# Performance work log

Hardware: AMD Instinct MI355X
Metric: run time of the kernel (lower is better)

## Reference

```python
import jax, jax.numpy as jnp
import numpy as np

D = 1024
H = 16
DH = D // H  # 64


def setup_inputs() -> dict:
    key = jax.random.key(0)
    ks = jax.random.split(key, 11)
    B, S = 2, 2048
    s = 1.0 / np.sqrt(D)  # torch Linear default init scale (uniform bound)
    mk = lambda k, shape: jax.random.uniform(k, shape, jnp.float32, -s, s)
    return {
        "q": jax.random.normal(ks[0], (B, S, D), jnp.float32),
        "k": jax.random.normal(ks[1], (B, S, D), jnp.float32),
        "v": jax.random.normal(ks[2], (B, S, D), jnp.float32),
        "Wq": mk(ks[3], (D, D)), "bq": mk(ks[4], (D,)),
        "Wk": mk(ks[5], (D, D)), "bk": mk(ks[6], (D,)),
        "Wv": mk(ks[7], (D, D)), "bv": mk(ks[8], (D,)),
        "Wo": mk(ks[9], (D, D)), "bo": mk(ks[10], (D,)),
    }


def reference(q, k, v, Wq, bq, Wk, bk, Wv, bv, Wo, bo):
    B, S, _ = q.shape
    scaling = DH ** (-0.5)
    # torch Linear: x @ W.T + b ; then split heads -> (B, H, S, DH)
    split = lambda x: x.reshape(B, -1, H, DH).transpose(0, 2, 1, 3)
    Q = split(q @ Wq.T + bq)
    K = split(k @ Wk.T + bk)
    V = split(v @ Wv.T + bv)
    scores = jnp.einsum("bhqd,bhkd->bhqk", Q, K) * scaling  # [B,H,S,S]
    attn = jax.nn.softmax(scores, axis=-1)
    out = jnp.einsum("bhqk,bhkd->bhqd", attn, V)
    out = out.transpose(0, 2, 1, 3).reshape(B, S, D)
    return out @ Wo.T + bo
```

## Files before the change

### kernel.cpp

```cpp
#include <hip/hip_runtime.h>
#include <stdint.h>

#define DIM   1024
#define HEADS 16
#define DHEAD 64
#define SEQ   2048
#define MROWS 4096
#define NQ    (MROWS * DIM)
#define NW    (DIM * DIM)

typedef unsigned short u16;
typedef __attribute__((ext_vector_type(8))) short short8;
typedef __attribute__((ext_vector_type(16))) float f32x16;

static_assert(sizeof(short8) == 16, "short8 must be 16B");

__device__ __forceinline__ float bf2f(u16 u) {
  union { float f; uint32_t u; } x; x.u = ((uint32_t)u) << 16; return x.f;
}
__device__ __forceinline__ u16 f2bf(float f) {
  union { float f; uint32_t u; } x; x.f = f;
  uint32_t r = x.u + 0x7FFFu + ((x.u >> 16) & 1u);
  return (u16)(r >> 16);
}
__device__ __forceinline__ float asf(uint32_t u) {
  union { float f; uint32_t u; } x; x.u = u; return x.f;
}
__device__ __forceinline__ uint32_t cvtpk(float lo, float hi) {
  uint32_t r;
  asm("v_cvt_pk_bf16_f32 %0, %1, %2" : "=v"(r) : "v"(lo), "v"(hi));
  return r;
}
__device__ __forceinline__ float exp2fast(float x) {
#if __has_builtin(__builtin_amdgcn_exp2f)
  return __builtin_amdgcn_exp2f(x);
#else
  return __expf(x * 0.69314718055994531f);
#endif
}

#if __has_builtin(__builtin_amdgcn_global_load_lds)
#define HAVE_GLLDS 1
#else
#define HAVE_GLLDS 0
#endif

__device__ __forceinline__ void stage16(const u16* src, u16* ldsbase, int cb, int lane) {
#if HAVE_GLLDS
  (void)lane;
  __builtin_amdgcn_global_load_lds((const __attribute__((address_space(1))) void*)src,
                                   (__attribute__((address_space(3))) void*)(ldsbase + (size_t)cb * 8),
                                   16, 0, 0);
#else
  *(short8*)(ldsbase + ((size_t)cb + lane) * 8) = *(const short8*)src;
#endif
}

__global__ __launch_bounds__(256)
void cvt_all(const float* __restrict__ q, const float* __restrict__ k, const float* __restrict__ v,
             const float* __restrict__ wq, const float* __restrict__ wk,
             const float* __restrict__ wv, const float* __restrict__ wo,
             u16* __restrict__ qc, u16* __restrict__ kc, u16* __restrict__ vc,
             u16* __restrict__ wqc, u16* __restrict__ wkc, u16* __restrict__ wvc, u16* __restrict__ woc)
{
  const float* s; u16* d; int n;
  switch (blockIdx.y) {
    case 0: s = q;  d = qc;  n = NQ; break;
    case 1: s = k;  d = kc;  n = NQ; break;
    case 2: s = v;  d = vc;  n = NQ; break;
    case 3: s = wq; d = wqc; n = NW; break;
    case 4: s = wk; d = wkc; n = NW; break;
    case 5: s = wv; d = wvc; n = NW; break;
    default: s = wo; d = woc; n = NW; break;
  }
  const int n8 = n >> 3;
  for (int i = blockIdx.x * blockDim.x + threadIdx.x; i < n8; i += gridDim.x * blockDim.x) {
    float4 f0 = ((const float4*)s)[2 * i];
    float4 f1 = ((const float4*)s)[2 * i + 1];
    union { uint32_t w[4]; short8 s8; } u;
    u.w[0] = cvtpk(f0.x, f0.y); u.w[1] = cvtpk(f0.z, f0.w);
    u.w[2] = cvtpk(f1.x, f1.y); u.w[3] = cvtpk(f1.z, f1.w);
    ((short8*)d)[i] = u.s8;
  }
}

__global__ __launch_bounds__(256)
void gemm_qkv(const u16* __restrict__ A0, const u16* __restrict__ W0, const float* __restrict__ b0, u16* __restrict__ O0, float s0_,
              const u16* __restrict__ A1, const u16* __restrict__ W1, const float* __restrict__ b1, u16* __restrict__ O1, float s1_,
              const u16* __restrict__ A2, const u16* __restrict__ W2, const float* __restrict__ b2, u16* __restrict__ O2, float s2_)
{
  constexpr int BM = 128, BN = 128, BK = 64;
  __shared__ u16 As[BM * BK];
  __shared__ u16 Bs[BN * BK];

  const u16* A = A0; const u16* W = W0; const float* bias = b0; u16* O = O0; float oscale = s0_;
  if (blockIdx.z == 1) { A = A1; W = W1; bias = b1; O = O1; oscale = s1_; }
  else if (blockIdx.z == 2) { A = A2; W = W2; bias = b2; O = O2; oscale = s2_; }

  const int tid  = threadIdx.x;
  const int wave = tid >> 6, lane = tid & 63;
  const int l31 = lane & 31, hi = lane >> 5;
  const int wr = wave >> 1, wc = wave & 1;
  const int bx = ((blockIdx.x & 7) << 2) | (blockIdx.x >> 3);
  const int m0 = bx * BM, n0 = blockIdx.y * BN;

  f32x16 acc[2][2];
  for (int mb = 0; mb < 2; ++mb)
    for (int nb = 0; nb < 2; ++nb)
      for (int r = 0; r < 16; ++r) acc[mb][nb][r] = 0.f;

  for (int k0 = 0; k0 < DIM; k0 += BK) {
    __syncthreads();
    constexpr int AI = (BM * 8) / 256;
    for (int i = 0; i < AI; ++i) {
      int cb = (wave * AI + i) * 64;
      int ch = cb + lane;
      int row = ch >> 3, kc = ch & 7;
      stage16(A + (size_t)(m0 + row) * DIM + k0 + (kc ^ (row & 7)) * 8, As, cb, lane);
    }
    constexpr int BI = (BN * 8) / 256;
    for (int i = 0; i < BI; ++i) {
      int cb = (wave * BI + i) * 64;
      int ch = cb + lane;
      int row = ch >> 3, kc = ch & 7;
      stage16(W + (size_t)(n0 + row) * DIM + k0 + (kc ^ (row & 7)) * 8, Bs, cb, lane);
    }
    __syncthreads();

    #pragma unroll
    for (int kk = 0; kk < 4; ++kk) {
      short8 af[2], bf[2];
      #pragma unroll
      for (int mb = 0; mb < 2; ++mb) {
        uint32_t row = (uint32_t)(wr * 64 + mb * 32 + l31);
        af[mb] = *(const short8*)((const char*)As +
                   (row * 128 + ((uint32_t)(kk * 32 + hi * 16) ^ ((row & 7) << 4))));
      }
      #pragma unroll
      for (int nb = 0; nb < 2; ++nb) {
        uint32_t row = (uint32_t)(wc * 64 + nb * 32 + l31);
        bf[nb] = *(const short8*)((const char*)Bs +
                   (row * 128 + ((uint32_t)(kk * 32 + hi * 16) ^ ((row & 7) << 4))));
      }
      __builtin_amdgcn_s_setprio(1);
      #pragma unroll
      for (int mb = 0; mb < 2; ++mb)
        #pragma unroll
        for (int nb = 0; nb < 2; ++nb)
          acc[mb][nb] = __builtin_amdgcn_mfma_f32_32x32x16_bf16(af[mb], bf[nb], acc[mb][nb], 0, 0, 0);
      __builtin_amdgcn_s_setprio(0);
    }
  }

  for (int nb = 0; nb < 2; ++nb) {
    int col = n0 + wc * 64 + nb * 32 + l31;
    float bv = bias[col];
    int hh = col >> 6, dh = col & 63;
    for (int mb = 0; mb < 2; ++mb) {
      int rowb = m0 + wr * 64 + mb * 32 + hi * 4;
      for (int r = 0; r < 16; ++r) {
        int row = rowb + (r & 3) + ((r >> 2) << 3);
        float val = (acc[mb][nb][r] + bv) * oscale;
        int b = row >> 11, s = row & (SEQ - 1);
        O[((((size_t)b * HEADS + hh) * SEQ + s) << 6) + dh] = f2bf(val);
      }
    }
  }
}

__global__ __launch_bounds__(256)
void gemm_out(const u16* __restrict__ Op0, const u16* __restrict__ Op1,
              const float* __restrict__ lstats, const u16* __restrict__ W,
              const float* __restrict__ bias, float* __restrict__ Out)
{
  constexpr int BM = 64, BN = 128, BK = 64;
  __shared__ u16 As[BM * BK];
  __shared__ u16 Bs[BN * BK];
  __shared__ float wtab[HEADS * BM];

  const int tid  = threadIdx.x;
  const int wave = tid >> 6, lane = tid & 63;
  const int l31 = lane & 31, hi = lane >> 5;
  const int wr = wave >> 1, wc = wave & 1;
  const int bx = ((blockIdx.x & 7) << 3) | (blockIdx.x >> 3);
  const int m0 = bx * BM, n0 = blockIdx.y * BN;

  for (int e = tid; e < HEADS * BM; e += 256) {
    int h = e >> 6, r = e & 63;
    int row = m0 + r;
    int b = row >> 11, s = row & (SEQ - 1);
    float l0 = lstats[(size_t)(b * 16 + h) * SEQ + s];
    float l1 = lstats[(size_t)(32 + b * 16 + h) * SEQ + s];
    wtab[e] = 1.0f / (l0 + l1);
  }

  f32x16 acc[2];
  for (int nb = 0; nb < 2; ++nb)
    for (int r = 0; r < 16; ++r) acc[nb][r] = 0.f;

  for (int k0 = 0; k0 < DIM; k0 += BK) {
    __syncthreads();
    const int h = k0 >> 6;
    constexpr int AI = (BM * 8) / 256;
    #pragma unroll
    for (int i = 0; i < AI; ++i) {
      int ch = (wave * AI + i) * 64 + lane;
      int row = ch >> 3, kc = ch & 7;
      int grow = m0 + row;
      int b = grow >> 11, s = grow & (SEQ - 1);
      size_t off = ((size_t)(b * 16 + h) * SEQ + s) * 64 + kc * 8;
      short8 a8 = *(const short8*)(Op0 + off);
      short8 b8 = *(const short8*)(Op1 + off);
      float winv = wtab[h * BM + row];
      union { uint32_t w[4]; short8 s8; } u;
      const uint32_t* wa = (const uint32_t*)&a8;
      const uint32_t* wb = (const uint32_t*)&b8;
      #pragma unroll
      for (int j = 0; j < 4; ++j) {
        float lo = (asf(wa[j] << 16) + asf(wb[j] << 16)) * winv;
        float hi2 = (asf(wa[j] & 0xffff0000u) + asf(wb[j] & 0xffff0000u)) * winv;
        u.w[j] = cvtpk(lo, hi2);
      }
      *(short8*)((char*)As + (((uint32_t)row * 128 + (uint32_t)kc * 16) ^ (((uint32_t)row & 7) << 4))) = u.s8;
    }
    constexpr int BI = (BN * 8) / 256;
    for (int i = 0; i < BI; ++i) {
      int cb = (wave * BI + i) * 64;
      int ch = cb + lane;
      int row = ch >> 3, kc = ch & 7;
      stage16(W + (size_t)(n0 + row) * DIM + k0 + (kc ^ (row & 7)) * 8, Bs, cb, lane);
    }
    __syncthreads();

    #pragma unroll
    for (int kk = 0; kk < 4; ++kk) {
      short8 af, bf[2];
      {
        uint32_t row = (uint32_t)(wr * 32 + l31);
        af = *(const short8*)((const char*)As +
               (row * 128 + ((uint32_t)(kk * 32 + hi * 16) ^ ((row & 7) << 4))));
      }
      #pragma unroll
      for (int nb = 0; nb < 2; ++nb) {
        uint32_t row = (uint32_t)(wc * 64 + nb * 32 + l31);
        bf[nb] = *(const short8*)((const char*)Bs +
                   (row * 128 + ((uint32_t)(kk * 32 + hi * 16) ^ ((row & 7) << 4))));
      }
      __builtin_amdgcn_s_setprio(1);
      #pragma unroll
      for (int nb = 0; nb < 2; ++nb)
        acc[nb] = __builtin_amdgcn_mfma_f32_32x32x16_bf16(af, bf[nb], acc[nb], 0, 0, 0);
      __builtin_amdgcn_s_setprio(0);
    }
  }

  for (int nb = 0; nb < 2; ++nb) {
    int col = n0 + wc * 64 + nb * 32 + l31;
    float bv = bias[col];
    int rowb = m0 + wr * 32 + hi * 4;
    for (int r = 0; r < 16; ++r) {
      int row = rowb + (r & 3) + ((r >> 2) << 3);
      Out[(size_t)row * DIM + col] = acc[nb][r] + bv;
    }
  }
}

#if __has_builtin(__builtin_amdgcn_permlane32_swap)
typedef __attribute__((ext_vector_type(2))) unsigned uint2v;
#define REPACK(PF, A_, B_, C_, D_)                                             \
  {                                                                            \
    uint2v w02 = __builtin_amdgcn_permlane32_swap((A_), (C_), false, false);   \
    uint2v w13 = __builtin_amdgcn_permlane32_swap((B_), (D_), false, false);   \
    union { uint32_t w[4]; short8 s8; } u_;                                    \
    u_.w[0] = w02[0]; u_.w[1] = w13[0]; u_.w[2] = w02[1]; u_.w[3] = w13[1];    \
    PF = u_.s8;                                                                \
  }
#else
#define REPACK(PF, A_, B_, C_, D_)                                             \
  {                                                                            \
    uint32_t pa = __shfl_xor((int)(A_), 32), pb = __shfl_xor((int)(B_), 32);   \
    uint32_t pc = __shfl_xor((int)(C_), 32), pd = __shfl_xor((int)(D_), 32);   \
    union { uint32_t w[4]; short8 s8; } u_;                                    \
    u_.w[0] = hi ? pc : (A_); u_.w[1] = hi ? pd : (B_);                        \
    u_.w[2] = hi ? (C_) : pa; u_.w[3] = hi ? (D_) : pb;                        \
    PF = u_.s8;                                                                \
  }
#endif

#define PV_BLOCK(SS, KSB)                                                      \
  {                                                                            \
    uint32_t a  = cvtpk(SS[0], SS[1]),   b3 = cvtpk(SS[2], SS[3]);             \
    uint32_t c  = cvtpk(SS[4], SS[5]),   d  = cvtpk(SS[6], SS[7]);             \
    uint32_t e  = cvtpk(SS[8], SS[9]),   f  = cvtpk(SS[10], SS[11]);           \
    uint32_t g2 = cvtpk(SS[12], SS[13]), h2 = cvtpk(SS[14], SS[15]);           \
    short8 pf0, pf1;                                                           \
    REPACK(pf0, a, b3, c, d)                                                   \
    REPACK(pf1, e, f, g2, h2)                                                  \
    uint32_t kvb0 = (uint32_t)((KSB) * 64 + hi * 16), kvb1 = kvb0 + 32;        \
    uint32_t r0 = (uint32_t)l31, r1 = 32u + (uint32_t)l31;                     \
    uint32_t sw = ((uint32_t)l31 & 7) << 4;                                    \
    short8 vf00 = *(const short8*)(Vc + ((r0 * 128 + kvb0) ^ sw));             \
    short8 vf01 = *(const short8*)(Vc + ((r1 * 128 + kvb0) ^ sw));             \
    short8 vf10 = *(const short8*)(Vc + ((r0 * 128 + kvb1) ^ sw));             \
    short8 vf11 = *(const short8*)(Vc + ((r1 * 128 + kvb1) ^ sw));             \
    __builtin_amdgcn_s_setprio(1);                                             \
    o0   = __builtin_amdgcn_mfma_f32_32x32x16_bf16(vf00, pf0, o0, 0, 0, 0);    \
    o1   = __builtin_amdgcn_mfma_f32_32x32x16_bf16(vf01, pf0, o1, 0, 0, 0);    \
    accL = __builtin_amdgcn_mfma_f32_32x32x16_bf16(ones8, pf0, accL, 0, 0, 0); \
    o0   = __builtin_amdgcn_mfma_f32_32x32x16_bf16(vf10, pf1, o0, 0, 0, 0);    \
    o1   = __builtin_amdgcn_mfma_f32_32x32x16_bf16(vf11, pf1, o1, 0, 0, 0);    \
    accL = __builtin_amdgcn_mfma_f32_32x32x16_bf16(ones8, pf1, accL, 0, 0, 0); \
    __builtin_amdgcn_s_setprio(0);                                             \
  }

__global__ __launch_bounds__(256)
void attn_fwd7(const u16* __restrict__ Qb, const u16* __restrict__ Kb,
               const u16* __restrict__ Vb, u16* __restrict__ Opart,
               float* __restrict__ lstats)
{
  uint32_t lid = blockIdx.x;
  uint32_t logical = (lid & 7) * 128 + (lid >> 3);
  const int qt    = logical & 15;
  const int bh    = (logical >> 4) & 31;
  const int split = logical >> 9;

  const int q0 = qt * 128;
  const int kvbase = split * (SEQ / 2);
  const int tid = threadIdx.x, wave = tid >> 6, lane = tid & 63;
  const int l31 = lane & 31, hi = lane >> 5;

  const size_t base = (size_t)bh * SEQ * DHEAD;
  const u16* Qg = Qb + base;
  const u16* Kg = Kb + base;
  const u16* Vg = Vb + base;

  __shared__ u16 Ks[2][64 * 64];
  __shared__ u16 Vts[2][64 * 64];

  const short8 ones8 = {0x3F80, 0x3F80, 0x3F80, 0x3F80,
                        0x3F80, 0x3F80, 0x3F80, 0x3F80};

  short8 qf[4];
  {
    const u16* qrow = Qg + (size_t)(q0 + wave * 32 + l31) * DHEAD + hi * 8;
    for (int ks = 0; ks < 4; ++ks)
      qf[ks] = *(const short8*)(qrow + ks * 16);
  }

  f32x16 o0, o1, accL;
  for (int r = 0; r < 16; ++r) { o0[r] = 0.f; o1[r] = 0.f; accL[r] = 0.f; }

  const int rp = tid & 31, c8 = tid >> 5;
  const int kr = tid >> 3, kc0 = tid & 7;
  short8 ka, kb2, va, vb2;

  const u16* pKa = Kg + (size_t)(kvbase + kr) * DHEAD + kc0 * 8;
  const u16* pKb = pKa + 32 * DHEAD;
  const u16* pVa = Vg + (size_t)(kvbase + 2 * rp) * DHEAD + c8 * 8;
  const u16* pVb = pVa + DHEAD;

  {
    ka  = *(const short8*)pKa;
    kb2 = *(const short8*)pKb;
    va  = *(const short8*)pVa;
    vb2 = *(const short8*)pVb;
    uint32_t sw = ((uint32_t)kr & 7) << 4;
    *(short8*)((char*)Ks[0] + (((uint32_t)kr * 128 + (uint32_t)kc0 * 16) ^ sw)) = ka;
    *(short8*)((char*)Ks[0] + ((((uint32_t)kr + 32) * 128 + (uint32_t)kc0 * 16) ^ sw)) = kb2;
    for (int j = 0; j < 8; ++j) {
      uint32_t row = c8 * 8 + j;
      uint32_t byte = (row * 128 + rp * 4) ^ ((row & 7) << 4);
      *(uint32_t*)((char*)Vts[0] + byte) =
          (uint32_t)(u16)va[j] | ((uint32_t)(u16)vb2[j] << 16);
    }
  }
  __syncthreads();

  for (int t = 0; t < 16; ++t) {
    const int cur = t & 1;
    if (t < 15) {
      pKa += 64 * DHEAD; pKb += 64 * DHEAD;
      pVa += 64 * DHEAD; pVb += 64 * DHEAD;
      ka  = *(const short8*)pKa;
      kb2 = *(const short8*)pKb;
      va  = *(const short8*)pVa;
      vb2 = *(const short8*)pVb;
    }

    const char* Kc = (const char*)Ks[cur];
    const char* Vc = (const char*)Vts[cur];

    f32x16 s0, s1;
    for (int r = 0; r < 16; ++r) { s0[r] = 0.f; s1[r] = 0.f; }
    {
      uint32_t rb0 = (uint32_t)l31 * 128, sw0 = ((uint32_t)l31 & 7) << 4;
      uint32_t cbyte = (uint32_t)hi * 16;
      short8 k0 = *(const short8*)(Kc + ((rb0 + cbyte     ) ^ sw0));
      short8 k1 = *(const short8*)(Kc + ((rb0 + cbyte + 32) ^ sw0));
      short8 k2 = *(const short8*)(Kc + ((rb0 + cbyte + 64) ^ sw0));
      short8 k3 = *(const short8*)(Kc + ((rb0 + cbyte + 96) ^ sw0));
      uint32_t rb1 = rb0 + 32 * 128;
      short8 k4 = *(const short8*)(Kc + ((rb1 + cbyte     ) ^ sw0));
      short8 k5 = *(const short8*)(Kc + ((rb1 + cbyte + 32) ^ sw0));
      short8 k6 = *(const short8*)(Kc + ((rb1 + cbyte + 64) ^ sw0));
      short8 k7 = *(const short8*)(Kc + ((rb1 + cbyte + 96) ^ sw0));
      __builtin_amdgcn_s_setprio(1);
      s0 = __builtin_amdgcn_mfma_f32_32x32x16_bf16(k0, qf[0], s0, 0, 0, 0);
      s0 = __builtin_amdgcn_mfma_f32_32x32x16_bf16(k1, qf[1], s0, 0, 0, 0);
      s0 = __builtin_amdgcn_mfma_f32_32x32x16_bf16(k2, qf[2], s0, 0, 0, 0);
      s0 = __builtin_amdgcn_mfma_f32_32x32x16_bf16(k3, qf[3], s0, 0, 0, 0);
      s1 = __builtin_amdgcn_mfma_f32_32x32x16_bf16(k4, qf[0], s1, 0, 0, 0);
      s1 = __builtin_amdgcn_mfma_f32_32x32x16_bf16(k5, qf[1], s1, 0, 0, 0);
      s1 = __builtin_amdgcn_mfma_f32_32x32x16_bf16(k6, qf[2], s1, 0, 0, 0);
      s1 = __builtin_amdgcn_mfma_f32_32x32x16_bf16(k7, qf[3], s1, 0, 0, 0);
      __builtin_amdgcn_s_setprio(0);
    }

    for (int r = 0; r < 16; ++r) s0[r] = exp2fast(s0[r]);
    for (int r = 0; r < 16; ++r) s1[r] = exp2fast(s1[r]);

    PV_BLOCK(s0, 0)
    PV_BLOCK(s1, 1)

    if (t < 15) {
      uint32_t sw = ((uint32_t)kr & 7) << 4;
      char* Kn = (char*)Ks[cur ^ 1];
      *(short8*)(Kn + (((uint32_t)kr * 128 + (uint32_t)kc0 * 16) ^ sw)) = ka;
      *(short8*)(Kn + ((((uint32_t)kr + 32) * 128 + (uint32_t)kc0 * 16) ^ sw)) = kb2;
      char* Vn = (char*)Vts[cur ^ 1];
      for (int j = 0; j < 8; ++j) {
        uint32_t row = c8 * 8 + j;
        uint32_t byte = (row * 128 + rp * 4) ^ ((row & 7) << 4);
        *(uint32_t*)(Vn + byte) =
            (uint32_t)(u16)va[j] | ((uint32_t)(u16)vb2[j] << 16);
      }
      __syncthreads();
    }
  }

  const int q = q0 + wave * 32 + l31;
  u16* orow = Opart + (((size_t)split * 32 + bh) * SEQ + q) * DHEAD;
  for (int db = 0; db < 2; ++db) {
    const f32x16& o = db ? o1 : o0;
    for (int gq = 0; gq < 4; ++gq) {
      int dh = db * 32 + gq * 8 + hi * 4;
      ushort4 w;
      w.x = f2bf(o[gq * 4 + 0]); w.y = f2bf(o[gq * 4 + 1]);
      w.z = f2bf(o[gq * 4 + 2]); w.w = f2bf(o[gq * 4 + 3]);
      *(ushort4*)(orow + dh) = w;
    }
  }
  if (hi == 0)
    lstats[((size_t)split * 32 + bh) * SEQ + q] = accL[0];
}

extern "C" void kernel_launch(void* const* d_in, const int* in_sizes, int n_in,
                              void* d_out, int out_size, void* d_ws, size_t ws_size,
                              hipStream_t stream)
{
  const float* q  = (const float*)d_in[0];
  const float* k  = (const float*)d_in[1];
  const float* v  = (const float*)d_in[2];
  const float* Wq = (const float*)d_in[3];
  const float* bq = (const float*)d_in[4];
  const float* Wk = (const float*)d_in[5];
  const float* bk = (const float*)d_in[6];
  const float* Wv = (const float*)d_in[7];
  const float* bv = (const float*)d_in[8];
  const float* Wo = (const float*)d_in[9];
  const float* bo = (const float*)d_in[10];
  float* out = (float*)d_out;

  u16* qc  = (u16*)d_ws;
  u16* kc  = qc  + NQ;
  u16* vc  = kc  + NQ;
  u16* wqc = vc  + NQ;
  u16* wkc = wqc + NW;
  u16* wvc = wkc + NW;
  u16* woc = wvc + NW;
  u16* Qh  = woc + NW;
  u16* Kh  = Qh  + NQ;
  u16* Vh  = Kh  + NQ;

  u16* Op0 = (u16*)d_ws;
  u16* Op1 = Op0 + NQ;
  float* lstats = (float*)(Op1 + NQ);

  dim3 blk(256);
  hipLaunchKernelGGL(cvt_all, dim3(512, 7, 1), blk, 0, stream,
                     q, k, v, Wq, Wk, Wv, Wo, qc, kc, vc, wqc, wkc, wvc, woc);
  hipLaunchKernelGGL(gemm_qkv, dim3(MROWS / 128, DIM / 128, 3), blk, 0, stream,
                     qc, wqc, bq, Qh, 0.125f * 1.4426950408889634f,
                     kc, wkc, bk, Kh, 1.0f,
                     vc, wvc, bv, Vh, 1.0f);
  hipLaunchKernelGGL(attn_fwd7, dim3(1024, 1, 1), blk, 0, stream, Qh, Kh, Vh, Op0, lstats);
  hipLaunchKernelGGL(gemm_out, dim3(MROWS / 64, DIM / 128, 1), blk, 0, stream,
                     Op0, Op1, lstats, woc, bo, out);
}
```

Baseline: 125.3 us.

## Fuse fp32-to-bf16 activation conversion into the QKV projection GEMM

Activation conversion is removed from the standalone convert kernel; only the weights are still converted there. The QKV GEMM now stages fp32 activation tiles into LDS and converts them to bf16 when building MFMA fragments. This avoids writing and re-reading bf16 copies of q, k and v. In exchange, the GEMM loads twice as many activation bytes, uses more LDS (which may lower occupancy), and adds conversion ALU work in the inner loop. The workspace layout is reorganized so the attention outputs no longer alias the old conversion buffers.

```diff
diff --git a/kernel.cpp b/kernel.cpp
--- a/kernel.cpp
+++ b/kernel.cpp
@@ -55,25 +55,31 @@
   *(short8*)(ldsbase + ((size_t)cb + lane) * 8) = *(const short8*)src;
 #endif
 }
+__device__ __forceinline__ void stage16f(const float* src, float* ldsbase, int cb, int lane) {
+#if HAVE_GLLDS
+  (void)lane;
+  __builtin_amdgcn_global_load_lds((const __attribute__((address_space(1))) void*)src,
+                                   (__attribute__((address_space(3))) void*)(ldsbase + (size_t)cb * 4),
+                                   16, 0, 0);
+#else
+  *(float4*)(ldsbase + ((size_t)cb + lane) * 4) = *(const float4*)src;
+#endif
+}
 
 __global__ __launch_bounds__(256)
-void cvt_all(const float* __restrict__ q, const float* __restrict__ k, const float* __restrict__ v,
-             const float* __restrict__ wq, const float* __restrict__ wk,
-             const float* __restrict__ wv, const float* __restrict__ wo,
-             u16* __restrict__ qc, u16* __restrict__ kc, u16* __restrict__ vc,
-             u16* __restrict__ wqc, u16* __restrict__ wkc, u16* __restrict__ wvc, u16* __restrict__ woc)
+void cvt_w(const float* __restrict__ wq, const float* __restrict__ wk,
+           const float* __restrict__ wv, const float* __restrict__ wo,
+           u16* __restrict__ wqc, u16* __restrict__ wkc,
+           u16* __restrict__ wvc, u16* __restrict__ woc)
 {
-  const float* s; u16* d; int n;
+  const float* s; u16* d;
   switch (blockIdx.y) {
-    case 0: s = q;  d = qc;  n = NQ; break;
-    case 1: s = k;  d = kc;  n = NQ; break;
-    case 2: s = v;  d = vc;  n = NQ; break;
-    case 3: s = wq; d = wqc; n = NW; break;
-    case 4: s = wk; d = wkc; n = NW; break;
-    case 5: s = wv; d = wvc; n = NW; break;
-    default: s = wo; d = woc; n = NW; break;
-  }
-  const int n8 = n >> 3;
+    case 0: s = wq; d = wqc; break;
+    case 1: s = wk; d = wkc; break;
+    case 2: s = wv; d = wvc; break;
+    default: s = wo; d = woc; break;
+  }
+  const int n8 = NW >> 3;
   for (int i = blockIdx.x * blockDim.x + threadIdx.x; i < n8; i += gridDim.x * blockDim.x) {
     float4 f0 = ((const float4*)s)[2 * i];
     float4 f1 = ((const float4*)s)[2 * i + 1];
@@ -85,15 +91,15 @@
 }
 
 __global__ __launch_bounds__(256)
-void gemm_qkv(const u16* __restrict__ A0, const u16* __restrict__ W0, const float* __restrict__ b0, u16* __restrict__ O0, float s0_,
-              const u16* __restrict__ A1, const u16* __restrict__ W1, const float* __restrict__ b1, u16* __restrict__ O1, float s1_,
-              const u16* __restrict__ A2, const u16* __restrict__ W2, const float* __restrict__ b2, u16* __restrict__ O2, float s2_)
+void gemm_qkv(const float* __restrict__ A0, const u16* __restrict__ W0, const float* __restrict__ b0, u16* __restrict__ O0, float s0_,
+              const float* __restrict__ A1, const u16* __restrict__ W1, const float* __restrict__ b1, u16* __restrict__ O1, float s1_,
+              const float* __restrict__ A2, const u16* __restrict__ W2, const float* __restrict__ b2, u16* __restrict__ O2, float s2_)
 {
   constexpr int BM = 128, BN = 128, BK = 64;
-  __shared__ u16 As[BM * BK];
-  __shared__ u16 Bs[BN * BK];
-
-  const u16* A = A0; const u16* W = W0; const float* bias = b0; u16* O = O0; float oscale = s0_;
+  __shared__ float Asf[BM * BK];
+  __shared__ u16   Bs[BN * BK];
+
+  const float* A = A0; const u16* W = W0; const float* bias = b0; u16* O = O0; float oscale = s0_;
   if (blockIdx.z == 1) { A = A1; W = W1; bias = b1; O = O1; oscale = s1_; }
   else if (blockIdx.z == 2) { A = A2; W = W2; bias = b2; O = O2; oscale = s2_; }
 
@@ -111,12 +117,12 @@
 
   for (int k0 = 0; k0 < DIM; k0 += BK) {
     __syncthreads();
-    constexpr int AI = (BM * 8) / 256;
-    for (int i = 0; i < AI; ++i) {
-      int cb = (wave * AI + i) * 64;
+    constexpr int AIF = (BM * 16) / 256;
+    for (int i = 0; i < AIF; ++i) {
+      int cb = (wave * AIF + i) * 64;
       int ch = cb + lane;
-      int row = ch >> 3, kc = ch & 7;
-      stage16(A + (size_t)(m0 + row) * DIM + k0 + (kc ^ (row & 7)) * 8, As, cb, lane);
+      int row = ch >> 4, kc = ch & 15;
+      stage16f(A + (size_t)(m0 + row) * DIM + k0 + (kc ^ (row & 7)) * 4, Asf, cb, lane);
     }
     constexpr int BI = (BN * 8) / 256;
     for (int i = 0; i < BI; ++i) {
@@ -133,8 +139,14 @@
       #pragma unroll
       for (int mb = 0; mb < 2; ++mb) {
         uint32_t row = (uint32_t)(wr * 64 + mb * 32 + l31);
-        af[mb] = *(const short8*)((const char*)As +
-                   (row * 128 + ((uint32_t)(kk * 32 + hi * 16) ^ ((row & 7) << 4))));
+        uint32_t sw = (row & 7) << 4;
+        uint32_t base = row * 256 + (uint32_t)(kk * 64 + hi * 32);
+        float4 f0 = *(const float4*)((const char*)Asf + ((base     ) ^ sw));
+        float4 f1 = *(const float4*)((const char*)Asf + ((base + 16) ^ sw));
+        union { uint32_t w[4]; short8 s8; } u;
+        u.w[0] = cvtpk(f0.x, f0.y); u.w[1] = cvtpk(f0.z, f0.w);
+        u.w[2] = cvtpk(f1.x, f1.y); u.w[3] = cvtpk(f1.z, f1.w);
+        af[mb] = u.s8;
       }
       #pragma unroll
       for (int nb = 0; nb < 2; ++nb) {
@@ -471,28 +483,24 @@
   const float* bo = (const float*)d_in[10];
   float* out = (float*)d_out;
 
-  u16* qc  = (u16*)d_ws;
-  u16* kc  = qc  + NQ;
-  u16* vc  = kc  + NQ;
-  u16* wqc = vc  + NQ;
+  u16* wqc = (u16*)d_ws;
   u16* wkc = wqc + NW;
   u16* wvc = wkc + NW;
   u16* woc = wvc + NW;
   u16* Qh  = woc + NW;
   u16* Kh  = Qh  + NQ;
   u16* Vh  = Kh  + NQ;
-
-  u16* Op0 = (u16*)d_ws;
+  u16* Op0 = Vh  + NQ;
   u16* Op1 = Op0 + NQ;
   float* lstats = (float*)(Op1 + NQ);
 
   dim3 blk(256);
-  hipLaunchKernelGGL(cvt_all, dim3(512, 7, 1), blk, 0, stream,
-                     q, k, v, Wq, Wk, Wv, Wo, qc, kc, vc, wqc, wkc, wvc, woc);
+  hipLaunchKernelGGL(cvt_w, dim3(256, 4, 1), blk, 0, stream,
+                     Wq, Wk, Wv, Wo, wqc, wkc, wvc, woc);
   hipLaunchKernelGGL(gemm_qkv, dim3(MROWS / 128, DIM / 128, 3), blk, 0, stream,
-                     qc, wqc, bq, Qh, 0.125f * 1.4426950408889634f,
-                     kc, wkc, bk, Kh, 1.0f,
-                     vc, wvc, bv, Vh, 1.0f);
+                     q, wqc, bq, Qh, 0.125f * 1.4426950408889634f,
+                     k, wkc, bk, Kh, 1.0f,
+                     v, wvc, bv, Vh, 1.0f);
   hipLaunchKernelGGL(attn_fwd7, dim3(1024, 1, 1), blk, 0, stream, Qh, Kh, Vh, Op0, lstats);
   hipLaunchKernelGGL(gemm_out, dim3(MROWS / 64, DIM / 128, 1), blk, 0, stream,
                      Op0, Op1, lstats, woc, bo, out);
```

Result: slower. 132.8 us (+6.0%).
